# Kernel optimization log

Hardware: AMD Instinct MI355X
Metric: run time of the kernel (lower is better)

## Reference

```python
import jax, jax.numpy as jnp
import numpy as np

K = 4        # maximum_fertility + 1
OOV_ID = 1
HIDDEN = 512


def setup_inputs() -> dict:
    key = jax.random.key(0)
    ks = jax.random.split(key, 8)
    B, S, D, E, H, V = 4, 128, 512, 256, HIDDEN, 32000
    return {
        "embedded_input": jax.random.normal(ks[0], (B, S, D), jnp.float32),
        "input_mask": jnp.ones((B, S), jnp.int32),
        "emb_table": jax.random.normal(ks[1], (V, E), jnp.float32) * 0.02,
        "W_ih": jax.random.normal(ks[2], (4 * H, D + E), jnp.float32) * 0.02,
        "b_ih": jax.random.normal(ks[3], (4 * H,), jnp.float32) * 0.02,
        "W_hh": jax.random.normal(ks[4], (4 * H, H), jnp.float32) * 0.02,
        "b_hh": jax.random.normal(ks[5], (4 * H,), jnp.float32) * 0.02,
        "W_out": jax.random.normal(ks[6], (V, H), jnp.float32) * 0.02,
        "b_out": jax.random.normal(ks[7], (V,), jnp.float32) * 0.02,
    }


def reference(embedded_input, input_mask, emb_table, W_ih, b_ih, W_hh, b_hh, W_out, b_out):
    B, S, D = embedded_input.shape
    V, E = emb_table.shape
    H = HIDDEN
    N = B * S
    x = embedded_input.reshape(N, D)                      # (N, D)
    h0 = jnp.zeros((N, H), embedded_input.dtype)
    c0 = jnp.zeros((N, H), embedded_input.dtype)
    # initial last_output: one-hot at OOV id (prob mass 1.0 on oov)
    last0 = jnp.zeros((N, V), embedded_input.dtype).at[:, OOV_ID].set(1.0)

    def step(carry, _):
        h, c, last = carry
        # embedding_bag soft mix over full vocab == weighted sum == matmul
        emb_last = last @ emb_table                        # (N, E)
        inp = jnp.concatenate([x, emb_last], axis=1)       # (N, D+E)
        gates = inp @ W_ih.T + b_ih + h @ W_hh.T + b_hh    # (N, 4H)
        i, f, g, o = jnp.split(gates, 4, axis=1)           # torch LSTMCell gate order
        i = jax.nn.sigmoid(i)
        f = jax.nn.sigmoid(f)
        g = jnp.tanh(g)
        o = jax.nn.sigmoid(o)
        c_new = f * c + i * g
        h_new = o * jnp.tanh(c_new)
        # dropout=0 / eval -> dropout mask is all ones (no-op)
        logits = h_new @ W_out.T + b_out                   # (N, V)
        logp = jax.nn.log_softmax(logits, axis=-1)
        return (h_new, c_new, jnp.exp(logp)), logp

    _, outs = jax.lax.scan(step, (h0, c0, last0), None, length=K)  # (K, N, V)
    return outs.transpose(1, 0, 2).reshape(B, S, K, V)
```

## Files before the change

kernel.cpp:

```cpp
#include <hip/hip_runtime.h>
#include <hip/hip_bf16.h>
#include <math.h>

#define N_ROWS 512
#define D_IN   512
#define E_EMB  256
#define H_DIM  512
#define G_DIM  2048
#define V_DIM  32000
#define IN_LD  1280
#define KG     768
#define K_STEPS 4
#define OOV_ID 1
#define TBK 64
#define EMB_SPLIT 100
#define EMB_CHUNK 320
#define SEGSTRIDE 512

typedef __attribute__((ext_vector_type(4))) float f32x4;
typedef __attribute__((ext_vector_type(8))) short bf16x8;
typedef __attribute__((ext_vector_type(8))) _Float16 f16x8;

__device__ inline short f2b(float v) {
    __hip_bfloat16 h = __float2bfloat16(v);
    return *reinterpret_cast<short*>(&h);
}

__device__ inline void gload_lds(const short* g, short* l) {
    __builtin_amdgcn_global_load_lds(
        (const __attribute__((address_space(1))) void*)g,
        (__attribute__((address_space(3))) void*)l, 16, 0, 0);
}

template<int TBM, int TBN, int WR_, int WC_, int MODE, int INITC>
__global__ __launch_bounds__(WR_ * WC_ * 64) void k_gemm(
    const short* __restrict__ A, int lda,
    const short* __restrict__ B, int ldb,
    const float* __restrict__ bias,
    float* __restrict__ C, size_t ldc, int Kc,
    float2* __restrict__ stats,
    float* __restrict__ cstate, short* __restrict__ hdst)
{
    constexpr int NW = WR_ * WC_;
    constexpr int WMT = TBM / WR_, WNT = TBN / WC_;
    constexpr int WM = WMT / 16, WN = WNT / 16;
    __shared__ short As[TBM * 64];
    __shared__ short Bs[TBN * 64];
    const int tid = threadIdx.x;
    const int lane = tid & 63, wid = tid >> 6;
    const int wr = wid % WR_, wc = wid / WR_;
    const int quad = lane >> 4, l16 = lane & 15;
    const int m0 = blockIdx.y * TBM, n0 = blockIdx.x * TBN;
    const int kbase = blockIdx.z * Kc;
    const int lrow = lane >> 3;
    const int lsw  = ((lane & 7) ^ lrow) * 8;

    f32x4 acc[WM][WN];
    if constexpr (INITC) {
#pragma unroll
        for (int i = 0; i < WM; ++i)
#pragma unroll
            for (int j = 0; j < WN; ++j) {
                const int n = n0 + wc * WNT + j * 16 + l16;
#pragma unroll
                for (int r = 0; r < 4; ++r) {
                    const int m = m0 + wr * WMT + i * 16 + quad * 4 + r;
                    acc[i][j][r] = C[(size_t)m * ldc + n];
                }
            }
    } else {
#pragma unroll
        for (int i = 0; i < WM; ++i)
#pragma unroll
            for (int j = 0; j < WN; ++j)
#pragma unroll
                for (int r = 0; r < 4; ++r) acc[i][j][r] = 0.0f;
    }

    for (int kt = 0; kt < Kc; kt += TBK) {
        const int k0 = kbase + kt;
#pragma unroll
        for (int ch = wid; ch < TBM / 8; ch += NW)
            gload_lds(&A[(size_t)(m0 + ch * 8 + lrow) * lda + k0 + lsw], &As[ch * 512]);
#pragma unroll
        for (int ch = wid; ch < TBN / 8; ch += NW)
            gload_lds(&B[(size_t)(n0 + ch * 8 + lrow) * ldb + k0 + lsw], &Bs[ch * 512]);
        __syncthreads();
#pragma unroll
        for (int ks = 0; ks < 2; ++ks) {
            bf16x8 af[WM], bfv[WN];
#pragma unroll
            for (int i = 0; i < WM; ++i) {
                int rr = wr * WMT + i * 16 + l16;
                af[i] = *(const bf16x8*)&As[rr * 64 + (((ks * 4 + quad) ^ (l16 & 7)) * 8)];
            }
#pragma unroll
            for (int j = 0; j < WN; ++j) {
                int rr = wc * WNT + j * 16 + l16;
                bfv[j] = *(const bf16x8*)&Bs[rr * 64 + (((ks * 4 + quad) ^ (l16 & 7)) * 8)];
            }
#pragma unroll
            for (int i = 0; i < WM; ++i)
#pragma unroll
                for (int j = 0; j < WN; ++j)
                    acc[i][j] = __builtin_amdgcn_mfma_f32_16x16x32_bf16(af[i], bfv[j], acc[i][j], 0, 0, 0);
        }
        __syncthreads();
    }

    if constexpr (MODE == 3) {
        float* Cp = C + (size_t)blockIdx.z * N_ROWS * ldc;
#pragma unroll
        for (int i = 0; i < WM; ++i)
#pragma unroll
            for (int j = 0; j < WN; ++j) {
                const int n = n0 + wc * WNT + j * 16 + l16;
#pragma unroll
                for (int r = 0; r < 4; ++r) {
                    const int m = m0 + wr * WMT + i * 16 + quad * 4 + r;
                    Cp[(size_t)m * ldc + n] = acc[i][j][r];
                }
            }
    } else if constexpr (MODE == 2) {
        float bv[WN];
#pragma unroll
        for (int j = 0; j < WN; ++j) bv[j] = INITC ? 0.0f : bias[n0 + j * 16 + l16];
        const int jj = (n0 >> 2) + l16;
#pragma unroll
        for (int i = 0; i < WM; ++i) {
#pragma unroll
            for (int r = 0; r < 4; ++r) {
                const int m = m0 + wr * WMT + i * 16 + quad * 4 + r;
                float gi = acc[i][0][r] + bv[0];
                float gf = acc[i][1][r] + bv[1];
                float gg = acc[i][2][r] + bv[2];
                float go = acc[i][3][r] + bv[3];
                float i_ = 1.0f / (1.0f + expf(-gi));
                float f_ = 1.0f / (1.0f + expf(-gf));
                float g_ = tanhf(gg);
                float o_ = 1.0f / (1.0f + expf(-go));
                const size_t ci = (size_t)m * H_DIM + jj;
                float cn = f_ * cstate[ci] + i_ * g_;
                cstate[ci] = cn;
                hdst[(size_t)m * IN_LD + (D_IN + E_EMB) + jj] = f2b(o_ * tanhf(cn));
            }
        }
    } else if constexpr (MODE == 4) {
        _Float16* Ch = (_Float16*)C;
        float bv[WN];
#pragma unroll
        for (int j = 0; j < WN; ++j) bv[j] = bias[n0 + wc * WNT + j * 16 + l16];
#pragma unroll
        for (int i = 0; i < WM; ++i) {
            float rm[4] = {-1e30f, -1e30f, -1e30f, -1e30f};
            float rs[4] = {0.f, 0.f, 0.f, 0.f};
#pragma unroll
            for (int j = 0; j < WN; ++j)
#pragma unroll
                for (int r = 0; r < 4; ++r)
                    rm[r] = fmaxf(rm[r], acc[i][j][r] + bv[j]);
#pragma unroll
            for (int j = 0; j < WN; ++j) {
                const int n = n0 + wc * WNT + j * 16 + l16;
#pragma unroll
                for (int r = 0; r < 4; ++r) {
                    const int m = m0 + wr * WMT + i * 16 + quad * 4 + r;
                    float z = acc[i][j][r] + bv[j];
                    rs[r] += __expf(z - rm[r]);
                    Ch[(size_t)m * ldc + n] = (_Float16)z;
                }
            }
#pragma unroll
            for (int mask = 1; mask < 16; mask <<= 1) {
#pragma unroll
                for (int r = 0; r < 4; ++r) {
                    float om = __shfl_xor(rm[r], mask);
                    float os = __shfl_xor(rs[r], mask);
                    float nm = fmaxf(rm[r], om);
                    rs[r] = rs[r] * __expf(rm[r] - nm) + os * __expf(om - nm);
                    rm[r] = nm;
                }
            }
            if (l16 == 0) {
                const int seg = (n0 + wc * WNT) >> 6;
#pragma unroll
                for (int r = 0; r < 4; ++r) {
                    const int m = m0 + wr * WMT + i * 16 + quad * 4 + r;
                    stats[(size_t)m * SEGSTRIDE + seg] = make_float2(rm[r], rs[r]);
                }
            }
        }
    } else {
        float bv[WN];
#pragma unroll
        for (int j = 0; j < WN; ++j) bv[j] = bias[n0 + wc * WNT + j * 16 + l16];
#pragma unroll
        for (int i = 0; i < WM; ++i)
#pragma unroll
            for (int j = 0; j < WN; ++j) {
                const int n = n0 + wc * WNT + j * 16 + l16;
#pragma unroll
                for (int r = 0; r < 4; ++r) {
                    const int m = m0 + wr * WMT + i * 16 + quad * 4 + r;
                    C[(size_t)m * ldc + n] = acc[i][j][r] + bv[j];
                }
            }
    }
}

__global__ __launch_bounds__(256) void k_prep(
    const float* __restrict__ x, const float* __restrict__ emb_table,
    const float* __restrict__ W_ih, const float* __restrict__ W_hh,
    const float* __restrict__ b_ih, const float* __restrict__ b_hh,
    const float* __restrict__ W_out,
    short* __restrict__ Abuf, short* __restrict__ Wg, short* __restrict__ Wx16,
    float* __restrict__ bsum, short* __restrict__ Wout16, float* __restrict__ c)
{
    const int idx0 = blockIdx.x * 256 + threadIdx.x;
    const int gs = gridDim.x * 256;
    const float4* W4 = (const float4*)W_out;
    for (int i = idx0; i < V_DIM * H_DIM / 4; i += gs) {
        float4 v = W4[i];
        short4 o;
        o.x = f2b(v.x); o.y = f2b(v.y); o.z = f2b(v.z); o.w = f2b(v.w);
        ((short4*)Wout16)[i] = o;
    }
    for (int i = idx0; i < G_DIM * KG; i += gs) {
        int rp = i / KG, k = i - rp * KG;
        int j = ((rp >> 6) << 4) | (rp & 15);
        int gate = (rp >> 4) & 3;
        int g = gate * H_DIM + j;
        float v = (k < E_EMB) ? W_ih[(size_t)g * (D_IN + E_EMB) + D_IN + k]
                              : W_hh[(size_t)g * H_DIM + (k - E_EMB)];
        Wg[i] = f2b(v);
    }
    for (int i = idx0; i < G_DIM * D_IN; i += gs) {
        int rp = i / D_IN, k = i - rp * D_IN;
        int j = ((rp >> 6) << 4) | (rp & 15);
        int gate = (rp >> 4) & 3;
        int g = gate * H_DIM + j;
        Wx16[i] = f2b(W_ih[(size_t)g * (D_IN + E_EMB) + k]);
    }
    for (int i = idx0; i < G_DIM; i += gs) {
        int j = ((i >> 6) << 4) | (i & 15);
        int gate = (i >> 4) & 3;
        int g = gate * H_DIM + j;
        bsum[i] = b_ih[g] + b_hh[g];
    }
    for (int i = idx0; i < N_ROWS * IN_LD; i += gs) {
        int n = i / IN_LD, col = i - n * IN_LD;
        float v;
        if (col < D_IN)              v = x[(size_t)n * D_IN + col];
        else if (col < D_IN + E_EMB) v = emb_table[(size_t)OOV_ID * E_EMB + (col - D_IN)];
        else                         v = 0.0f;
        Abuf[i] = f2b(v);
    }
    for (int i = idx0; i < N_ROWS * H_DIM; i += gs) c[i] = 0.0f;
}

__global__ __launch_bounds__(256) void k_trans(const float* __restrict__ emb,
                                               short* __restrict__ embT)
{
    __shared__ float tile[64][65];
    const int v0 = blockIdx.x * 64, e0 = blockIdx.y * 64;
    const int tid = threadIdx.x;
#pragma unroll
    for (int i = 0; i < 16; ++i) {
        int idx = tid + i * 256;
        int vr = idx >> 6, ec = idx & 63;
        tile[vr][ec] = emb[(size_t)(v0 + vr) * E_EMB + e0 + ec];
    }
    __syncthreads();
#pragma unroll
    for (int i = 0; i < 16; ++i) {
        int idx = tid + i * 256;
        int er = idx >> 6, vc = idx & 63;
        embT[(size_t)(e0 + er) * V_DIM + v0 + vc] = f2b(tile[vc][er]);
    }
}

__global__ __launch_bounds__(256) void k_embred(const float* __restrict__ ep,
                                                short* __restrict__ Abuf)
{
    int idx = blockIdx.x * 256 + threadIdx.x;
    int n = idx >> 8, e = idx & 255;
    float s0 = 0.f, s1 = 0.f;
#pragma unroll 2
    for (int z = 0; z < EMB_SPLIT; z += 2) {
        s0 += ep[((size_t)z * N_ROWS + n) * E_EMB + e];
        s1 += ep[((size_t)(z + 1) * N_ROWS + n) * E_EMB + e];
    }
    Abuf[(size_t)n * IN_LD + D_IN + e] = f2b(s0 + s1);
}

__global__ __launch_bounds__(256) void k_lse(const float2* __restrict__ stats,
                                             float* __restrict__ lse)
{
    const int tid = threadIdx.x;
    const int lane = tid & 63, wid = tid >> 6;
    const int n = blockIdx.x * 4 + wid;

    float m = -1e30f, s = 0.0f;
    for (int sg = lane; sg < V_DIM / 64; sg += 64) {
        float2 p = stats[(size_t)n * SEGSTRIDE + sg];
        float nm = fmaxf(m, p.x);
        s = s * __expf(m - nm) + p.y * __expf(p.x - nm);
        m = nm;
    }
#pragma unroll
    for (int mask = 32; mask > 0; mask >>= 1) {
        float om = __shfl_xor(m, mask);
        float os = __shfl_xor(s, mask);
        float nm = fmaxf(m, om);
        s = s * __expf(m - nm) + os * __expf(om - nm);
        m = nm;
    }
    if (lane == 0) lse[n] = m + __logf(s);
}

__global__ __launch_bounds__(256) void k_finish(const _Float16* __restrict__ zbuf,
                                                float* __restrict__ out,
                                                short* __restrict__ last,
                                                const float* __restrict__ lse,
                                                int step, int feed)
{
    const int n = blockIdx.y;
    const float l = lse[n];
    const f16x8* zr = (const f16x8*)(zbuf + (size_t)n * V_DIM);
    float4* row4 = (float4*)(out + ((size_t)n * K_STEPS + step) * V_DIM);
    bf16x8* prow = (bf16x8*)(last + (size_t)n * V_DIM);
#pragma unroll
    for (int it = 0; it < 2; ++it) {
        const int slot = threadIdx.x + it * 256;
        if (slot < 500) {
            const int cidx = blockIdx.x * 500 + slot;
            f16x8 zv = zr[cidx];
            float lp[8];
#pragma unroll
            for (int k = 0; k < 8; ++k) lp[k] = (float)zv[k] - l;
            row4[cidx * 2]     = make_float4(lp[0], lp[1], lp[2], lp[3]);
            row4[cidx * 2 + 1] = make_float4(lp[4], lp[5], lp[6], lp[7]);
            if (feed) {
                bf16x8 p;
#pragma unroll
                for (int k = 0; k < 8; ++k) p[k] = f2b(__expf(lp[k]));
                prow[cidx] = p;
            }
        }
    }
}

extern "C" void kernel_launch(void* const* d_in, const int* in_sizes, int n_in,
                              void* d_out, int out_size, void* d_ws, size_t ws_size,
                              hipStream_t stream) {
    (void)in_sizes; (void)n_in; (void)out_size; (void)ws_size;
    const float* x       = (const float*)d_in[0];
    const float* emb_tab = (const float*)d_in[2];
    const float* W_ih    = (const float*)d_in[3];
    const float* b_ih    = (const float*)d_in[4];
    const float* W_hh    = (const float*)d_in[5];
    const float* b_hh    = (const float*)d_in[6];
    const float* W_out   = (const float*)d_in[7];
    const float* b_out   = (const float*)d_in[8];
    float* out = (float*)d_out;

    char* ws = (char*)d_ws;
    short* Abuf   = (short*)ws;  ws += (size_t)N_ROWS * IN_LD * sizeof(short);
    float* c      = (float*)ws;  ws += (size_t)N_ROWS * H_DIM * sizeof(float);
    short* last   = (short*)ws;  ws += (size_t)N_ROWS * V_DIM * sizeof(short);
    short* Wout16 = (short*)ws;  ws += (size_t)V_DIM * H_DIM * sizeof(short);
    short* Wg     = (short*)ws;  ws += (size_t)G_DIM * KG * sizeof(short);
    short* Wx16   = (short*)ws;  ws += (size_t)G_DIM * D_IN * sizeof(short);
    float* bsum   = (float*)ws;  ws += (size_t)G_DIM * sizeof(float);
    float* gates0 = (float*)ws;  ws += (size_t)N_ROWS * G_DIM * sizeof(float);
    short* embT   = (short*)ws;  ws += (size_t)E_EMB * V_DIM * sizeof(short);
    float2* stats = (float2*)ws; ws += (size_t)N_ROWS * SEGSTRIDE * sizeof(float2);
    float* lse    = (float*)ws;  ws += (size_t)N_ROWS * sizeof(float);
    ws = (char*)(((size_t)ws + 255) & ~(size_t)255);
    _Float16* zbuf = (_Float16*)ws;
    float* epart   = (float*)ws;
    ws += (size_t)EMB_SPLIT * N_ROWS * E_EMB * sizeof(float);

    k_prep<<<2048, 256, 0, stream>>>(x, emb_tab, W_ih, W_hh, b_ih, b_hh, W_out,
                                     Abuf, Wg, Wx16, bsum, Wout16, c);
    k_trans<<<dim3(V_DIM / 64, E_EMB / 64), 256, 0, stream>>>(emb_tab, embT);
    k_gemm<64, 64, 4, 1, 0, 0><<<dim3(G_DIM / 64, N_ROWS / 64, 1), 256, 0, stream>>>(
        Abuf, IN_LD, Wx16, D_IN, bsum, gates0, G_DIM, D_IN, nullptr, nullptr, nullptr);

    for (int t = 0; t < K_STEPS; ++t) {
        if (t > 0) {
            k_gemm<128, 256, 2, 4, 3, 0><<<dim3(1, N_ROWS / 128, EMB_SPLIT), 512, 0, stream>>>(
                last, V_DIM, embT, V_DIM, nullptr, epart, E_EMB, EMB_CHUNK,
                nullptr, nullptr, nullptr);
            k_embred<<<N_ROWS * E_EMB / 256, 256, 0, stream>>>(epart, Abuf);
        }
        k_gemm<64, 64, 4, 1, 2, 1><<<dim3(G_DIM / 64, N_ROWS / 64, 1), 256, 0, stream>>>(
            Abuf + D_IN, IN_LD, Wg, KG, nullptr, gates0, G_DIM, KG, nullptr, c, Abuf);
        k_gemm<256, 128, 4, 2, 4, 0><<<dim3(V_DIM / 128, N_ROWS / 256, 1), 512, 0, stream>>>(
            Abuf + (D_IN + E_EMB), IN_LD, Wout16, H_DIM, b_out,
            (float*)zbuf, V_DIM, H_DIM, stats, nullptr, nullptr);
        const int feed = (t < K_STEPS - 1) ? 1 : 0;
        k_lse<<<N_ROWS / 4, 256, 0, stream>>>(stats, lse);
        k_finish<<<dim3(8, N_ROWS), 256, 0, stream>>>(zbuf, out, last, lse, t, feed);
    }
}
```

Baseline: 702.1 us.

## Fuse log-sum-exp into finish kernel and retune split and output GEMM tiles

Removes the separate k_lse launch: each k_finish block now reduces the per-segment max/sum stats itself, with a shared-memory cross-wave combine, before writing log-probs and probabilities. This drops one launch per step and the lse buffer, but the 500-segment reduction is repeated by each of the 8 blocks per row. The embedding split-K is halved (50 chunks of 640), which cuts partial-sum traffic and reduction work at the cost of fewer blocks. The vocab-projection GEMM moves from a 256x128 tile with 512 threads to 128x128 with 256 threads, doubling the grid.

```diff
diff --git a/kernel.cpp b/kernel.cpp
--- a/kernel.cpp
+++ b/kernel.cpp
@@ -13,8 +13,8 @@
 #define K_STEPS 4
 #define OOV_ID 1
 #define TBK 64
-#define EMB_SPLIT 100
-#define EMB_CHUNK 320
+#define EMB_SPLIT 50
+#define EMB_CHUNK 640
 #define SEGSTRIDE 512
 
 typedef __attribute__((ext_vector_type(4))) float f32x4;
@@ -293,45 +293,48 @@
     Abuf[(size_t)n * IN_LD + D_IN + e] = f2b(s0 + s1);
 }
 
-__global__ __launch_bounds__(256) void k_lse(const float2* __restrict__ stats,
-                                             float* __restrict__ lse)
+__global__ __launch_bounds__(256) void k_finish(const _Float16* __restrict__ zbuf,
+                                                float* __restrict__ out,
+                                                short* __restrict__ last,
+                                                const float2* __restrict__ stats,
+                                                int step, int feed)
 {
+    const int n = blockIdx.y;
     const int tid = threadIdx.x;
     const int lane = tid & 63, wid = tid >> 6;
-    const int n = blockIdx.x * 4 + wid;
+    __shared__ float redm[4], reds[4];
 
     float m = -1e30f, s = 0.0f;
-    for (int sg = lane; sg < V_DIM / 64; sg += 64) {
+    for (int sg = tid; sg < V_DIM / 64; sg += 256) {
         float2 p = stats[(size_t)n * SEGSTRIDE + sg];
         float nm = fmaxf(m, p.x);
         s = s * __expf(m - nm) + p.y * __expf(p.x - nm);
         m = nm;
     }
 #pragma unroll
-    for (int mask = 32; mask > 0; mask >>= 1) {
-        float om = __shfl_xor(m, mask);
-        float os = __shfl_xor(s, mask);
-        float nm = fmaxf(m, om);
-        s = s * __expf(m - nm) + os * __expf(om - nm);
+    for (int off = 32; off > 0; off >>= 1) {
+        float m2 = __shfl_down(m, off), s2 = __shfl_down(s, off);
+        float nm = fmaxf(m, m2);
+        s = s * __expf(m - nm) + s2 * __expf(m2 - nm);
         m = nm;
     }
-    if (lane == 0) lse[n] = m + __logf(s);
-}
-
-__global__ __launch_bounds__(256) void k_finish(const _Float16* __restrict__ zbuf,
-                                                float* __restrict__ out,
-                                                short* __restrict__ last,
-                                                const float* __restrict__ lse,
-                                                int step, int feed)
-{
-    const int n = blockIdx.y;
-    const float l = lse[n];
+    if (lane == 0) { redm[wid] = m; reds[wid] = s; }
+    __syncthreads();
+    float fm = redm[0], fs = reds[0];
+#pragma unroll
+    for (int w = 1; w < 4; ++w) {
+        float nm = fmaxf(fm, redm[w]);
+        fs = fs * __expf(fm - nm) + reds[w] * __expf(redm[w] - nm);
+        fm = nm;
+    }
+    const float l = fm + __logf(fs);
+
     const f16x8* zr = (const f16x8*)(zbuf + (size_t)n * V_DIM);
     float4* row4 = (float4*)(out + ((size_t)n * K_STEPS + step) * V_DIM);
     bf16x8* prow = (bf16x8*)(last + (size_t)n * V_DIM);
 #pragma unroll
     for (int it = 0; it < 2; ++it) {
-        const int slot = threadIdx.x + it * 256;
+        const int slot = tid + it * 256;
         if (slot < 500) {
             const int cidx = blockIdx.x * 500 + slot;
             f16x8 zv = zr[cidx];
@@ -375,7 +378,6 @@
     float* gates0 = (float*)ws;  ws += (size_t)N_ROWS * G_DIM * sizeof(float);
     short* embT   = (short*)ws;  ws += (size_t)E_EMB * V_DIM * sizeof(short);
     float2* stats = (float2*)ws; ws += (size_t)N_ROWS * SEGSTRIDE * sizeof(float2);
-    float* lse    = (float*)ws;  ws += (size_t)N_ROWS * sizeof(float);
     ws = (char*)(((size_t)ws + 255) & ~(size_t)255);
     _Float16* zbuf = (_Float16*)ws;
     float* epart   = (float*)ws;
@@ -396,11 +398,10 @@
         }
         k_gemm<64, 64, 4, 1, 2, 1><<<dim3(G_DIM / 64, N_ROWS / 64, 1), 256, 0, stream>>>(
             Abuf + D_IN, IN_LD, Wg, KG, nullptr, gates0, G_DIM, KG, nullptr, c, Abuf);
-        k_gemm<256, 128, 4, 2, 4, 0><<<dim3(V_DIM / 128, N_ROWS / 256, 1), 512, 0, stream>>>(
+        k_gemm<128, 128, 2, 2, 4, 0><<<dim3(V_DIM / 128, N_ROWS / 128, 1), 256, 0, stream>>>(
             Abuf + (D_IN + E_EMB), IN_LD, Wout16, H_DIM, b_out,
             (float*)zbuf, V_DIM, H_DIM, stats, nullptr, nullptr);
         const int feed = (t < K_STEPS - 1) ? 1 : 0;
-        k_lse<<<N_ROWS / 4, 256, 0, stream>>>(stats, lse);
-        k_finish<<<dim3(8, N_ROWS), 256, 0, stream>>>(zbuf, out, last, lse, t, feed);
-    }
-}
+        k_finish<<<dim3(8, N_ROWS), 256, 0, stream>>>(zbuf, out, last, stats, t, feed);
+    }
+}
```

New measurement: 717.5 us. 2.2% more time.
